# Kernel optimization log

Hardware: AMD Instinct MI355X
Metric: run time of the kernel (lower is better)

Reference implementation:

```python
import jax, jax.numpy as jnp
import numpy as np

REF_POSE = np.array([[213.33335876464844, 124.50563049316406], [190.504638671875, 115.11840057373047], [169.9791717529297, 101.77180480957031], [146.72341918945312, 96.25749206542969], [128.86770629882812, 87.2344970703125], [150.34292602539062, 101.61070251464844], [119.29926300048828, 98.73982238769531], [100.03463745117188, 99.74459838867188], [82.62400817871094, 101.2509536743164], [148.91049194335938, 112.71517181396484], [114.37303161621094, 113.20121002197266], [91.90096282958984, 116.49812316894531], [74.75020599365234, 119.37875366210938], [149.59658813476562, 124.09295654296875], [119.72419738769531, 126.36898040771484], [99.59107208251953, 129.40196228027344], [82.82524108886719, 131.584228515625], [154.55911254882812, 135.07681274414062], [133.8833770751953, 140.85983276367188], [120.45906066894531, 145.40306091308594], [106.21541595458984, 150.072265625]], dtype=np.float32)

SCALES = (0.25, 0.5, 1.0)
ORIENTATIONS = (0, 90, 180, 270)
INPUT_SIZE = (256, 256)          # (H, W)
ANCHOR_STRIDE = (1, 1)           # (y_stride, x_stride)
POS_TH = 0.5
KPT_SIGMA = 0.05                 # per-keypoint OKS falloff


def _generate_anchor_poses():
    # scale + rotate ref pose about its centroid -> [A, 21, 2]
    c = REF_POSE.mean(axis=0, keepdims=True)
    out = []
    for s in SCALES:
        for o in ORIENTATIONS:
            th = np.deg2rad(o)
            R = np.array([[np.cos(th), -np.sin(th)], [np.sin(th), np.cos(th)]], dtype=np.float32)
            out.append(c + s * (REF_POSE - c) @ R.T)
    return np.stack(out).astype(np.float32)


def _all_anchors(feat_h, feat_w):
    base = _generate_anchor_poses()                      # [A,21,2]
    w_ratio = INPUT_SIZE[1] / feat_w
    h_ratio = INPUT_SIZE[0] / feat_h
    sx = np.arange(0, feat_w, ANCHOR_STRIDE[1]) * w_ratio
    sy = np.arange(0, feat_h, ANCHOR_STRIDE[0]) * h_ratio
    gx, gy = np.meshgrid(sx, sy)
    shifts = np.stack([gx.ravel(), gy.ravel()], axis=1).astype(np.float32)  # [K,2]
    all_a = base[None, :, :, :] + shifts[:, None, None, :]                  # [K,A,21,2]
    return jnp.asarray(all_a.reshape(-1, 21, 2))                            # [K*A,21,2]


def _pose_oks(anchors, gt):
    # anchors [N,21,2], gt [B,2,21,3] -> OKS sim [B,N,2]
    d2 = jnp.sum((anchors[None, :, None, :, :] - gt[:, None, :, :, :2]) ** 2, axis=-1)  # [B,N,2,21]
    vis = (gt[..., 2] > 0).astype(anchors.dtype)[:, None, :, :]                          # [B,1,2,21]
    xy = gt[..., :2]
    area = jnp.prod(xy.max(axis=2) - xy.min(axis=2), axis=-1)                            # [B,2]
    s2 = jnp.maximum(area, 1.0)[:, None, :, None]                                        # [B,1,2,1]
    k2 = (2.0 * KPT_SIGMA) ** 2
    oks = jnp.exp(-d2 / (2.0 * s2 * k2))
    return jnp.sum(oks * vis, axis=-1) / jnp.maximum(jnp.sum(vis, axis=-1), 1.0)          # [B,N,2]


def setup_inputs() -> dict:
    key = jax.random.key(0)
    k1, k2 = jax.random.split(key)
    B = 16
    xy = jax.random.uniform(k1, (B, 42, 2), dtype=jnp.float32) * 216.0 + 20.0
    vis = jnp.ones((B, 42, 1), dtype=jnp.float32)
    pose_gt = jnp.concatenate([xy, vis], axis=-1)          # [B,42,3]
    hand_type = jnp.ones((B, 2), dtype=jnp.int32)          # both hands present
    return {"pose_gt": pose_gt, "hand_type": hand_type, "feat_h": 64, "feat_w": 64}


def reference(pose_gt, hand_type, feat_h, feat_w):
    all_anchors = _all_anchors(feat_h, feat_w)             # [N,21,2], N=K*A
    inside = jnp.sum((all_anchors[..., 0] >= 0) & (all_anchors[..., 1] >= 0)
                     & (all_anchors[..., 0] < INPUT_SIZE[0])
                     & (all_anchors[..., 1] < INPUT_SIZE[1]), axis=1) == 21  # [N]

    B = pose_gt.shape[0]
    gt = pose_gt.reshape(B, 2, 21, 3)                      # hand 0 = right, hand 1 = left
    sim = _pose_oks(all_anchors, gt)                       # [B,N,2]
    am = jnp.argmax(sim, axis=-1)                          # [B,N]
    mx = jnp.max(sim, axis=-1)                             # [B,N]

    right = (am == 0) & (mx > POS_TH) & (hand_type[:, 0:1] == 1) & inside[None, :]
    left = (am == 1) & (mx > POS_TH) & (hand_type[:, 1:2] == 1) & inside[None, :]
    neg = (~right) & (~left) & inside[None, :]

    # labels channel layout matches source: [:,:,0]=left, [:,:,1]=negative, [:,:,2]=right
    labels = jnp.stack([left, neg, right], axis=-1).astype(pose_gt.dtype)   # [B,N,3]
    labels = jnp.where(inside[None, :, None], labels, jnp.asarray(-1.0, pose_gt.dtype))

    pose_targets = (jnp.where(right[..., None, None], gt[:, 0][:, None], 0.0)
                    + jnp.where(left[..., None, None], gt[:, 1][:, None], 0.0))  # [B,N,21,3]

    offsets = pose_targets[..., :2] - all_anchors[None, :, :, :]             # [B,N,21,2]
    offsets = jnp.where(inside[None, :, None, None], offsets, 0.0)
    return all_anchors, inside, labels, offsets
```

## Files before the change

### kernel.cpp

```cpp
#include <hip/hip_runtime.h>
#include <math.h>

#define NA 49152
#define NB 16
#define ABLOCKS 192
#define LSTR 43
#define EPS 1e-3f

__constant__ float RP[21][2] = {
  {213.33335876464844f, 124.50563049316406f},
  {190.504638671875f,   115.11840057373047f},
  {169.9791717529297f,  101.77180480957031f},
  {146.72341918945312f, 96.25749206542969f},
  {128.86770629882812f, 87.2344970703125f},
  {150.34292602539062f, 101.61070251464844f},
  {119.29926300048828f, 98.73982238769531f},
  {100.03463745117188f, 99.74459838867188f},
  {82.62400817871094f,  101.2509536743164f},
  {148.91049194335938f, 112.71517181396484f},
  {114.37303161621094f, 113.20121002197266f},
  {91.90096282958984f,  116.49812316894531f},
  {74.75020599365234f,  119.37875366210938f},
  {149.59658813476562f, 124.09295654296875f},
  {119.72419738769531f, 126.36898040771484f},
  {99.59107208251953f,  129.40196228027344f},
  {82.82524108886719f,  131.584228515625f},
  {154.55911254882812f, 135.07681274414062f},
  {133.8833770751953f,  140.85983276367188f},
  {120.45906066894531f, 145.40306091308594f},
  {106.21541595458984f, 150.072265625f}
};

__device__ __forceinline__ void ref_center(float& cx, float& cy) {
  #pragma clang fp contract(off)
  float rx[8], ry[8];
  #pragma unroll
  for (int j = 0; j < 8; ++j) {
    rx[j] = RP[j][0] + RP[j + 8][0];
    ry[j] = RP[j][1] + RP[j + 8][1];
  }
  float sx = ((rx[0] + rx[1]) + (rx[2] + rx[3])) + ((rx[4] + rx[5]) + (rx[6] + rx[7]));
  float sy = ((ry[0] + ry[1]) + (ry[2] + ry[3])) + ((ry[4] + ry[5]) + (ry[6] + ry[7]));
  #pragma unroll
  for (int j = 16; j < 21; ++j) { sx += RP[j][0]; sy += RP[j][1]; }
  cx = sx / 21.0f;
  cy = sy / 21.0f;
}

__device__ __forceinline__ float2 anchor_pt(int p, int j, float cx, float cy,
                                            float shx, float shy) {
  #pragma clang fp contract(off)
  const int si = p >> 2, oi = p & 3;
  const float s = (si == 0) ? 0.25f : (si == 1 ? 0.5f : 1.0f);
  const float dx = s * (RP[j][0] - cx);
  const float dy = s * (RP[j][1] - cy);
  const float rx = (oi == 0) ? dx : (oi == 1 ? -dy : (oi == 2 ? -dx : dy));
  const float ry = (oi == 0) ? dy : (oi == 1 ? dx : (oi == 2 ? -dy : -dx));
  return make_float2((cx + rx) + shx, (cy + ry) + shy);
}

__global__ __launch_bounds__(256) void k_anchors(float* __restrict__ oa,
                                                 float* __restrict__ oinside) {
  __shared__ float sbuf[4 * 64 * LSTR];
  const int tid = threadIdx.x, lane = tid & 63, w = tid >> 6;
  float* wbuf = sbuf + w * (64 * LSTR);
  const int a = blockIdx.x * 256 + tid;
  float cx, cy; ref_center(cx, cy);
  const int p = a % 12;
  const int kc = a / 12;
  const float shx = 4.0f * (float)(kc & 63);
  const float shy = 4.0f * (float)(kc >> 6);
  bool inside = true;
  #pragma unroll
  for (int j = 0; j < 21; ++j) {
    float2 an = anchor_pt(p, j, cx, cy, shx, shy);
    inside = inside && (an.x >= 0.0f) && (an.y >= 0.0f) &&
                       (an.x < 256.0f) && (an.y < 256.0f);
    wbuf[lane * LSTR + 2 * j]     = an.x;
    wbuf[lane * LSTR + 2 * j + 1] = an.y;
  }
  oinside[a] = inside ? 1.0f : 0.0f;
  __syncthreads();
  const int a0 = blockIdx.x * 256 + w * 64;
  float2* op = reinterpret_cast<float2*>(oa) + (size_t)a0 * 21;
  #pragma unroll
  for (int i = 0; i < 21; ++i) {
    const int f2 = i * 64 + lane;
    const int aloc = f2 / 21;
    const int j = f2 - aloc * 21;
    op[f2] = make_float2(wbuf[aloc * LSTR + 2 * j],
                         wbuf[aloc * LSTR + 2 * j + 1]);
  }
}

__global__ __launch_bounds__(256) void k_targets(const float* __restrict__ gt,
                                                 const int* __restrict__ ht,
                                                 float* __restrict__ ol,
                                                 float* __restrict__ oo) {
  __shared__ float sbuf[4 * 64 * LSTR];
  __shared__ int shsel[256];
  __shared__ float sgt[126];
  __shared__ float sden[2];
  __shared__ float srden[2];
  __shared__ float snv[2];
  __shared__ int sht[2];
  const int tid = threadIdx.x, lane = tid & 63, w = tid >> 6;
  float* wbuf = sbuf + w * (64 * LSTR);
  const int b = blockIdx.x / ABLOCKS;
  const int ab = blockIdx.x % ABLOCKS;

  if (tid < 126) sgt[tid] = gt[b * 126 + tid];
  if (tid >= 128 && tid < 130) {
    const int h = tid - 128;
    const float* g = gt + b * 126 + h * 63;
    float mnx = g[0], mxx = g[0], mny = g[1], mxy = g[1];
    float nv = (g[2] > 0.0f) ? 1.0f : 0.0f;
    for (int j = 1; j < 21; ++j) {
      float x = g[j * 3], y = g[j * 3 + 1];
      mnx = fminf(mnx, x); mxx = fmaxf(mxx, x);
      mny = fminf(mny, y); mxy = fmaxf(mxy, y);
      nv += (g[j * 3 + 2] > 0.0f) ? 1.0f : 0.0f;
    }
    const float area = (mxx - mnx) * (mxy - mny);
    const float s2 = fmaxf(area, 1.0f);
    const float den = (2.0f * s2) * 0.01f;
    sden[h] = den;
    srden[h] = -1.0f / den;
    snv[h] = fmaxf(nv, 1.0f);
  }
  if (tid >= 130 && tid < 132) sht[tid - 130] = ht[b * 2 + (tid - 130)];
  __syncthreads();

  const int a = ab * 256 + tid;
  const int p = a % 12;
  const int kc = a / 12;
  const float shx = 4.0f * (float)(kc & 63);
  const float shy = 4.0f * (float)(kc >> 6);
  float cx, cy; ref_center(cx, cy);

  const float rd0 = srden[0], rd1 = srden[1];
  bool inside = true;
  float s0f = 0.0f, s1f = 0.0f;
  #pragma unroll
  for (int j = 0; j < 21; ++j) {
    float2 an = anchor_pt(p, j, cx, cy, shx, shy);
    inside = inside && (an.x >= 0.0f) && (an.y >= 0.0f) &&
                       (an.x < 256.0f) && (an.y < 256.0f);
    wbuf[lane * LSTR + 2 * j]     = an.x;
    wbuf[lane * LSTR + 2 * j + 1] = an.y;
    float dx0 = an.x - sgt[j * 3],      dy0 = an.y - sgt[j * 3 + 1];
    float dx1 = an.x - sgt[63 + j * 3], dy1 = an.y - sgt[63 + j * 3 + 1];
    float v0 = (sgt[j * 3 + 2] > 0.0f) ? 1.0f : 0.0f;
    float v1 = (sgt[63 + j * 3 + 2] > 0.0f) ? 1.0f : 0.0f;
    s0f += __expf((dx0 * dx0 + dy0 * dy0) * rd0) * v0;
    s1f += __expf((dx1 * dx1 + dy1 * dy1) * rd1) * v1;
  }
  float sim0 = s0f / snv[0];
  float sim1 = s1f / snv[1];
  const float mxf = fmaxf(sim0, sim1);
  const bool need_exact = (fabsf(mxf - 0.5f) < EPS) ||
                          ((mxf > 0.5f - EPS) && (fabsf(sim0 - sim1) < EPS));

  if (need_exact) {
    #pragma clang fp contract(off)
    float q0[8], q1[8];
    #pragma unroll
    for (int j = 0; j < 16; ++j) {
      float ax = wbuf[lane * LSTR + 2 * j], ay = wbuf[lane * LSTR + 2 * j + 1];
      float dx0 = ax - sgt[j * 3], dy0 = ay - sgt[j * 3 + 1];
      float d20 = dx0 * dx0 + dy0 * dy0;
      float vv0 = (sgt[j * 3 + 2] > 0.0f) ? 1.0f : 0.0f;
      float t0 = (float)::exp((double)(-d20 / sden[0])) * vv0;
      float dx1 = ax - sgt[63 + j * 3], dy1 = ay - sgt[63 + j * 3 + 1];
      float d21 = dx1 * dx1 + dy1 * dy1;
      float vv1 = (sgt[63 + j * 3 + 2] > 0.0f) ? 1.0f : 0.0f;
      float t1 = (float)::exp((double)(-d21 / sden[1])) * vv1;
      if (j < 8) { q0[j] = t0; q1[j] = t1; }
      else       { q0[j - 8] += t0; q1[j - 8] += t1; }
    }
    float s0 = ((q0[0] + q0[1]) + (q0[2] + q0[3])) + ((q0[4] + q0[5]) + (q0[6] + q0[7]));
    float s1 = ((q1[0] + q1[1]) + (q1[2] + q1[3])) + ((q1[4] + q1[5]) + (q1[6] + q1[7]));
    #pragma unroll
    for (int j = 16; j < 21; ++j) {
      float ax = wbuf[lane * LSTR + 2 * j], ay = wbuf[lane * LSTR + 2 * j + 1];
      float dx0 = ax - sgt[j * 3], dy0 = ay - sgt[j * 3 + 1];
      float d20 = dx0 * dx0 + dy0 * dy0;
      float vv0 = (sgt[j * 3 + 2] > 0.0f) ? 1.0f : 0.0f;
      s0 += (float)::exp((double)(-d20 / sden[0])) * vv0;
      float dx1 = ax - sgt[63 + j * 3], dy1 = ay - sgt[63 + j * 3 + 1];
      float d21 = dx1 * dx1 + dy1 * dy1;
      float vv1 = (sgt[63 + j * 3 + 2] > 0.0f) ? 1.0f : 0.0f;
      s1 += (float)::exp((double)(-d21 / sden[1])) * vv1;
    }
    sim0 = s0 / snv[0];
    sim1 = s1 / snv[1];
  }

  const int am = (sim1 > sim0) ? 1 : 0;
  const float mx = fmaxf(sim0, sim1);
  const bool pos = mx > 0.5f;
  const bool right = (am == 0) && pos && (sht[0] == 1) && inside;
  const bool left  = (am == 1) && pos && (sht[1] == 1) && inside;
  const bool neg   = (!right) && (!left) && inside;

  int c;
  if (!inside)      c = -1;
  else if (right)   c = 1;
  else if (left)    c = 2;
  else              c = 0;
  shsel[tid] = c;

  const size_t pidx = (size_t)b * NA + (size_t)a;
  float* lab = ol + pidx * 3;
  if (inside) {
    lab[0] = left ? 1.0f : 0.0f;
    lab[1] = neg  ? 1.0f : 0.0f;
    lab[2] = right ? 1.0f : 0.0f;
  } else {
    lab[0] = -1.0f; lab[1] = -1.0f; lab[2] = -1.0f;
  }

  __syncthreads();
  const int a0 = ab * 256 + w * 64;
  float2* op = reinterpret_cast<float2*>(oo) + ((size_t)b * NA + a0) * 21;
  #pragma unroll
  for (int i = 0; i < 21; ++i) {
    #pragma clang fp contract(off)
    const int f2 = i * 64 + lane;
    const int aloc = f2 / 21;
    const int j = f2 - aloc * 21;
    const float anx = wbuf[aloc * LSTR + 2 * j];
    const float any = wbuf[aloc * LSTR + 2 * j + 1];
    const int cc = shsel[w * 64 + aloc];
    const bool has = (cc == 1) || (cc == 2);
    const int hoff = (cc == 2) ? 63 : 0;
    const float tx = has ? sgt[hoff + j * 3]     : 0.0f;
    const float ty = has ? sgt[hoff + j * 3 + 1] : 0.0f;
    const float ox = (cc >= 0) ? (tx - anx) : 0.0f;
    const float oy = (cc >= 0) ? (ty - any) : 0.0f;
    op[f2] = make_float2(ox, oy);
  }
}

extern "C" void kernel_launch(void* const* d_in, const int* in_sizes, int n_in,
                              void* d_out, int out_size, void* d_ws, size_t ws_size,
                              hipStream_t stream) {
  (void)in_sizes; (void)n_in; (void)d_ws; (void)ws_size; (void)out_size;
  const float* gt = (const float*)d_in[0];
  const int* ht = (const int*)d_in[1];
  float* out = (float*)d_out;
  float* out_anchors = out;
  float* out_inside  = out + (size_t)NA * 42;
  float* out_labels  = out + (size_t)NA * 43;
  float* out_offsets = out_labels + (size_t)NB * NA * 3;

  hipLaunchKernelGGL(k_anchors, dim3(ABLOCKS), dim3(256), 0, stream,
                     out_anchors, out_inside);
  hipLaunchKernelGGL(k_targets, dim3(NB * ABLOCKS), dim3(256), 0, stream,
                     gt, ht, out_labels, out_offsets);
}
```

Baseline: 185.3 us.

## Fuse anchor and target kernels with shared base-pose table and float4 stores

Merges the anchor kernel into the target kernel, with batch-0 blocks writing the anchors and inside mask. The 252 base anchor points are computed once per block into a small shared table, replacing the large per-warp anchor staging buffer. Labels, offsets and anchors are now written as coalesced float4 stores, with anchors recomputed from the table plus the grid shift. This removes a launch and the big LDS footprint, which should raise occupancy, at the cost of extra integer division work per output element.

```diff
diff --git a/kernel.cpp b/kernel.cpp
--- a/kernel.cpp
+++ b/kernel.cpp
@@ -4,7 +4,6 @@
 #define NA 49152
 #define NB 16
 #define ABLOCKS 192
-#define LSTR 43
 #define EPS 1e-3f
 
 __constant__ float RP[21][2] = {
@@ -47,8 +46,7 @@
   cy = sy / 21.0f;
 }
 
-__device__ __forceinline__ float2 anchor_pt(int p, int j, float cx, float cy,
-                                            float shx, float shy) {
+__device__ __forceinline__ float2 base_pt(int p, int j, float cx, float cy) {
   #pragma clang fp contract(off)
   const int si = p >> 2, oi = p & 3;
   const float s = (si == 0) ? 0.25f : (si == 1 ? 0.5f : 1.0f);
@@ -56,62 +54,83 @@
   const float dy = s * (RP[j][1] - cy);
   const float rx = (oi == 0) ? dx : (oi == 1 ? -dy : (oi == 2 ? -dx : dy));
   const float ry = (oi == 0) ? dy : (oi == 1 ? dx : (oi == 2 ? -dy : -dx));
-  return make_float2((cx + rx) + shx, (cy + ry) + shy);
-}
-
-__global__ __launch_bounds__(256) void k_anchors(float* __restrict__ oa,
-                                                 float* __restrict__ oinside) {
-  __shared__ float sbuf[4 * 64 * LSTR];
-  const int tid = threadIdx.x, lane = tid & 63, w = tid >> 6;
-  float* wbuf = sbuf + w * (64 * LSTR);
-  const int a = blockIdx.x * 256 + tid;
-  float cx, cy; ref_center(cx, cy);
+  return make_float2(cx + rx, cy + ry);
+}
+
+__device__ __forceinline__ void dec_anchor(int f2, int a0, const float2* sb2,
+                                           float& anx, float& any,
+                                           int& aloc, int& j) {
+  #pragma clang fp contract(off)
+  aloc = f2 / 21;
+  j = f2 - aloc * 21;
+  const int a = a0 + aloc;
   const int p = a % 12;
   const int kc = a / 12;
   const float shx = 4.0f * (float)(kc & 63);
   const float shy = 4.0f * (float)(kc >> 6);
-  bool inside = true;
-  #pragma unroll
-  for (int j = 0; j < 21; ++j) {
-    float2 an = anchor_pt(p, j, cx, cy, shx, shy);
-    inside = inside && (an.x >= 0.0f) && (an.y >= 0.0f) &&
-                       (an.x < 256.0f) && (an.y < 256.0f);
-    wbuf[lane * LSTR + 2 * j]     = an.x;
-    wbuf[lane * LSTR + 2 * j + 1] = an.y;
-  }
-  oinside[a] = inside ? 1.0f : 0.0f;
-  __syncthreads();
-  const int a0 = blockIdx.x * 256 + w * 64;
-  float2* op = reinterpret_cast<float2*>(oa) + (size_t)a0 * 21;
-  #pragma unroll
-  for (int i = 0; i < 21; ++i) {
-    const int f2 = i * 64 + lane;
-    const int aloc = f2 / 21;
-    const int j = f2 - aloc * 21;
-    op[f2] = make_float2(wbuf[aloc * LSTR + 2 * j],
-                         wbuf[aloc * LSTR + 2 * j + 1]);
-  }
-}
-
-__global__ __launch_bounds__(256) void k_targets(const float* __restrict__ gt,
-                                                 const int* __restrict__ ht,
-                                                 float* __restrict__ ol,
-                                                 float* __restrict__ oo) {
-  __shared__ float sbuf[4 * 64 * LSTR];
+  const float2 bpv = sb2[p * 21 + j];
+  anx = bpv.x + shx;
+  any = bpv.y + shy;
+}
+
+__device__ __forceinline__ float4 off_quad(int idx, int a0, const float2* sb2,
+                                           const float* sgt, const int* shsel) {
+  #pragma clang fp contract(off)
+  float r[4];
+  #pragma unroll
+  for (int h = 0; h < 2; ++h) {
+    float anx, any; int aloc, j;
+    dec_anchor(idx * 2 + h, a0, sb2, anx, any, aloc, j);
+    const int cc = shsel[aloc];
+    const bool has = (cc == 1) || (cc == 2);
+    const int hoff = (cc == 2) ? 63 : 0;
+    const float tx = has ? sgt[hoff + j * 3] : 0.0f;
+    const float ty = has ? sgt[hoff + j * 3 + 1] : 0.0f;
+    r[h * 2]     = (cc >= 0) ? (tx - anx) : 0.0f;
+    r[h * 2 + 1] = (cc >= 0) ? (ty - any) : 0.0f;
+  }
+  return make_float4(r[0], r[1], r[2], r[3]);
+}
+
+__device__ __forceinline__ float4 anc_quad(int idx, int a0, const float2* sb2) {
+  float r[4];
+  #pragma unroll
+  for (int h = 0; h < 2; ++h) {
+    float anx, any; int aloc, j;
+    dec_anchor(idx * 2 + h, a0, sb2, anx, any, aloc, j);
+    r[h * 2] = anx;
+    r[h * 2 + 1] = any;
+  }
+  return make_float4(r[0], r[1], r[2], r[3]);
+}
+
+__global__ __launch_bounds__(256) void k_all(const float* __restrict__ gt,
+                                             const int* __restrict__ ht,
+                                             float* __restrict__ oa,
+                                             float* __restrict__ oins,
+                                             float* __restrict__ ol,
+                                             float* __restrict__ oo) {
+  __shared__ float2 sb2[252];
+  __shared__ float sgt[126];
+  __shared__ float sden[2], srden[2], snv[2];
+  __shared__ int sht[2];
   __shared__ int shsel[256];
-  __shared__ float sgt[126];
-  __shared__ float sden[2];
-  __shared__ float srden[2];
-  __shared__ float snv[2];
-  __shared__ int sht[2];
-  const int tid = threadIdx.x, lane = tid & 63, w = tid >> 6;
-  float* wbuf = sbuf + w * (64 * LSTR);
+  __shared__ float sins[256];
+
+  const int tid = threadIdx.x;
   const int b = blockIdx.x / ABLOCKS;
   const int ab = blockIdx.x % ABLOCKS;
+  const int a0 = ab * 256;
 
   if (tid < 126) sgt[tid] = gt[b * 126 + tid];
-  if (tid >= 128 && tid < 130) {
-    const int h = tid - 128;
+  if (tid < 252) {
+    float cx, cy; ref_center(cx, cy);
+    const int p = tid / 21;
+    const int j = tid - p * 21;
+    sb2[tid] = base_pt(p, j, cx, cy);
+  }
+  if (tid == 252 || tid == 253) {
+    const int h = tid - 252;
     const float* g = gt + b * 126 + h * 63;
     float mnx = g[0], mxx = g[0], mny = g[1], mxy = g[1];
     float nv = (g[2] > 0.0f) ? 1.0f : 0.0f;
@@ -128,30 +147,30 @@
     srden[h] = -1.0f / den;
     snv[h] = fmaxf(nv, 1.0f);
   }
-  if (tid >= 130 && tid < 132) sht[tid - 130] = ht[b * 2 + (tid - 130)];
+  if (tid == 254 || tid == 255) sht[tid - 254] = ht[b * 2 + (tid - 254)];
   __syncthreads();
 
-  const int a = ab * 256 + tid;
+  const int a = a0 + tid;
   const int p = a % 12;
   const int kc = a / 12;
   const float shx = 4.0f * (float)(kc & 63);
   const float shy = 4.0f * (float)(kc >> 6);
-  float cx, cy; ref_center(cx, cy);
+  const float2* bp = sb2 + p * 21;
 
   const float rd0 = srden[0], rd1 = srden[1];
   bool inside = true;
   float s0f = 0.0f, s1f = 0.0f;
   #pragma unroll
   for (int j = 0; j < 21; ++j) {
-    float2 an = anchor_pt(p, j, cx, cy, shx, shy);
-    inside = inside && (an.x >= 0.0f) && (an.y >= 0.0f) &&
-                       (an.x < 256.0f) && (an.y < 256.0f);
-    wbuf[lane * LSTR + 2 * j]     = an.x;
-    wbuf[lane * LSTR + 2 * j + 1] = an.y;
-    float dx0 = an.x - sgt[j * 3],      dy0 = an.y - sgt[j * 3 + 1];
-    float dx1 = an.x - sgt[63 + j * 3], dy1 = an.y - sgt[63 + j * 3 + 1];
-    float v0 = (sgt[j * 3 + 2] > 0.0f) ? 1.0f : 0.0f;
-    float v1 = (sgt[63 + j * 3 + 2] > 0.0f) ? 1.0f : 0.0f;
+    #pragma clang fp contract(off)
+    const float anx = bp[j].x + shx;
+    const float any = bp[j].y + shy;
+    inside = inside && (anx >= 0.0f) && (any >= 0.0f) &&
+                       (anx < 256.0f) && (any < 256.0f);
+    const float dx0 = anx - sgt[j * 3],      dy0 = any - sgt[j * 3 + 1];
+    const float dx1 = anx - sgt[63 + j * 3], dy1 = any - sgt[63 + j * 3 + 1];
+    const float v0 = (sgt[j * 3 + 2] > 0.0f) ? 1.0f : 0.0f;
+    const float v1 = (sgt[63 + j * 3 + 2] > 0.0f) ? 1.0f : 0.0f;
     s0f += __expf((dx0 * dx0 + dy0 * dy0) * rd0) * v0;
     s1f += __expf((dx1 * dx1 + dy1 * dy1) * rd1) * v1;
   }
@@ -166,7 +185,7 @@
     float q0[8], q1[8];
     #pragma unroll
     for (int j = 0; j < 16; ++j) {
-      float ax = wbuf[lane * LSTR + 2 * j], ay = wbuf[lane * LSTR + 2 * j + 1];
+      const float ax = bp[j].x + shx, ay = bp[j].y + shy;
       float dx0 = ax - sgt[j * 3], dy0 = ay - sgt[j * 3 + 1];
       float d20 = dx0 * dx0 + dy0 * dy0;
       float vv0 = (sgt[j * 3 + 2] > 0.0f) ? 1.0f : 0.0f;
@@ -182,7 +201,7 @@
     float s1 = ((q1[0] + q1[1]) + (q1[2] + q1[3])) + ((q1[4] + q1[5]) + (q1[6] + q1[7]));
     #pragma unroll
     for (int j = 16; j < 21; ++j) {
-      float ax = wbuf[lane * LSTR + 2 * j], ay = wbuf[lane * LSTR + 2 * j + 1];
+      const float ax = bp[j].x + shx, ay = bp[j].y + shy;
       float dx0 = ax - sgt[j * 3], dy0 = ay - sgt[j * 3 + 1];
       float d20 = dx0 * dx0 + dy0 * dy0;
       float vv0 = (sgt[j * 3 + 2] > 0.0f) ? 1.0f : 0.0f;
@@ -201,7 +220,6 @@
   const bool pos = mx > 0.5f;
   const bool right = (am == 0) && pos && (sht[0] == 1) && inside;
   const bool left  = (am == 1) && pos && (sht[1] == 1) && inside;
-  const bool neg   = (!right) && (!left) && inside;
 
   int c;
   if (!inside)      c = -1;
@@ -209,36 +227,57 @@
   else if (left)    c = 2;
   else              c = 0;
   shsel[tid] = c;
-
-  const size_t pidx = (size_t)b * NA + (size_t)a;
-  float* lab = ol + pidx * 3;
-  if (inside) {
-    lab[0] = left ? 1.0f : 0.0f;
-    lab[1] = neg  ? 1.0f : 0.0f;
-    lab[2] = right ? 1.0f : 0.0f;
-  } else {
-    lab[0] = -1.0f; lab[1] = -1.0f; lab[2] = -1.0f;
-  }
-
+  sins[tid] = inside ? 1.0f : 0.0f;
   __syncthreads();
-  const int a0 = ab * 256 + w * 64;
-  float2* op = reinterpret_cast<float2*>(oo) + ((size_t)b * NA + a0) * 21;
-  #pragma unroll
-  for (int i = 0; i < 21; ++i) {
-    #pragma clang fp contract(off)
-    const int f2 = i * 64 + lane;
-    const int aloc = f2 / 21;
-    const int j = f2 - aloc * 21;
-    const float anx = wbuf[aloc * LSTR + 2 * j];
-    const float any = wbuf[aloc * LSTR + 2 * j + 1];
-    const int cc = shsel[w * 64 + aloc];
-    const bool has = (cc == 1) || (cc == 2);
-    const int hoff = (cc == 2) ? 63 : 0;
-    const float tx = has ? sgt[hoff + j * 3]     : 0.0f;
-    const float ty = has ? sgt[hoff + j * 3 + 1] : 0.0f;
-    const float ox = (cc >= 0) ? (tx - anx) : 0.0f;
-    const float oy = (cc >= 0) ? (ty - any) : 0.0f;
-    op[f2] = make_float2(ox, oy);
+
+  if (tid < 192) {
+    float4* lf4 = reinterpret_cast<float4*>(ol + ((size_t)b * NA + a0) * 3);
+    float r[4];
+    #pragma unroll
+    for (int k = 0; k < 4; ++k) {
+      const int q = tid * 4 + k;
+      const int al = q / 3;
+      const int rr = q - al * 3;
+      const int cc = shsel[al];
+      float v;
+      if (cc < 0)       v = -1.0f;
+      else if (rr == 0) v = (cc == 2) ? 1.0f : 0.0f;
+      else if (rr == 1) v = (cc == 0) ? 1.0f : 0.0f;
+      else              v = (cc == 1) ? 1.0f : 0.0f;
+      r[k] = v;
+    }
+    lf4[tid] = make_float4(r[0], r[1], r[2], r[3]);
+  }
+
+  {
+    float4* of4 = reinterpret_cast<float4*>(oo + ((size_t)b * NA + a0) * 42);
+    #pragma unroll
+    for (int i = 0; i < 10; ++i) {
+      const int idx = i * 256 + tid;
+      of4[idx] = off_quad(idx, a0, sb2, sgt, shsel);
+    }
+    if (tid < 128) {
+      const int idx = 2560 + tid;
+      of4[idx] = off_quad(idx, a0, sb2, sgt, shsel);
+    }
+  }
+
+  if (b == 0) {
+    float4* af4 = reinterpret_cast<float4*>(oa + (size_t)a0 * 42);
+    #pragma unroll
+    for (int i = 0; i < 10; ++i) {
+      const int idx = i * 256 + tid;
+      af4[idx] = anc_quad(idx, a0, sb2);
+    }
+    if (tid < 128) {
+      const int idx = 2560 + tid;
+      af4[idx] = anc_quad(idx, a0, sb2);
+    }
+    if (tid < 64) {
+      float4* if4 = reinterpret_cast<float4*>(oins + a0);
+      if4[tid] = make_float4(sins[tid * 4], sins[tid * 4 + 1],
+                             sins[tid * 4 + 2], sins[tid * 4 + 3]);
+    }
   }
 }
 
@@ -254,8 +293,6 @@
   float* out_labels  = out + (size_t)NA * 43;
   float* out_offsets = out_labels + (size_t)NB * NA * 3;
 
-  hipLaunchKernelGGL(k_anchors, dim3(ABLOCKS), dim3(256), 0, stream,
-                     out_anchors, out_inside);
-  hipLaunchKernelGGL(k_targets, dim3(NB * ABLOCKS), dim3(256), 0, stream,
-                     gt, ht, out_labels, out_offsets);
-}
+  hipLaunchKernelGGL(k_all, dim3(NB * ABLOCKS), dim3(256), 0, stream,
+                     gt, ht, out_anchors, out_inside, out_labels, out_offsets);
+}
```

Measured after the change: 178.5 us. 1.04x faster.
